# Kernel optimization log

Measured on AMD Instinct MI355X. Metric: run time of the kernel, lower is better.

## Reference

```python
import jax, jax.numpy as jnp
import numpy as np

B, S, D, H = 2, 2048, 2048, 16
HD = D // H
FF = 4 * D
EPS = 1e-5
SCALE = 1.0 / np.sqrt(D)  # source uses 1/sqrt(d_out), not 1/sqrt(head_dim)


def _gelu_tanh(x):
    c = np.sqrt(2.0 / np.pi).astype(np.float32)
    return 0.5 * x * (1.0 + jnp.tanh(c * (x + 0.044715 * x * x * x)))


def _layernorm(x, scale, shift):
    mean = jnp.mean(x, axis=-1, keepdims=True)
    var = jnp.mean(jnp.square(x - mean), axis=-1, keepdims=True)  # correction=0
    return (x - mean) * jax.lax.rsqrt(var + EPS) * scale + shift


def setup_inputs() -> dict:
    key = jax.random.key(0)
    ks = jax.random.split(key, 10)
    init = lambda k, shape, fan_in: (jax.random.normal(k, shape, jnp.float32) / np.sqrt(fan_in))
    return {
        "x": jax.random.normal(ks[0], (B, S, D), jnp.float32),
        "wq": init(ks[1], (D, D), D),
        "wk": init(ks[2], (D, D), D),
        "wv": init(ks[3], (D, D), D),
        "wo": init(ks[4], (D, D), D),
        "bo": jnp.zeros((D,), jnp.float32),
        "g1": jnp.ones((D,), jnp.float32),
        "s1": jnp.zeros((D,), jnp.float32),
        "g2": jnp.ones((D,), jnp.float32),
        "s2": jnp.zeros((D,), jnp.float32),
        "w1": init(ks[5], (D, FF), D),
        "b1": jnp.zeros((FF,), jnp.float32),
        "w2": init(ks[6], (FF, D), FF),
        "b2": jnp.zeros((D,), jnp.float32),
    }


def _block(x, wq, wk, wv, wo, bo, g1, s1, g2, s2, w1, b1, w2, b2):
    # pre-LN attention
    h = _layernorm(x, g1, s1)
    q = (h @ wq).reshape(B, S, H, HD).transpose(0, 2, 1, 3)  # [B,H,S,HD]
    k = (h @ wk).reshape(B, S, H, HD).transpose(0, 2, 1, 3)
    v = (h @ wv).reshape(B, S, H, HD).transpose(0, 2, 1, 3)
    scores = jnp.einsum('bhqd,bhkd->bhqk', q, k) * SCALE
    causal = jnp.tril(jnp.ones((S, S), dtype=bool))  # mask strictly-upper
    scores = jnp.where(causal, scores, -jnp.inf)
    attn = jax.nn.softmax(scores, axis=-1)
    ctx = jnp.einsum('bhqk,bhkd->bhqd', attn, v)
    ctx = ctx.transpose(0, 2, 1, 3).reshape(B, S, D)
    x = x + ctx @ wo + bo
    # pre-LN FFN
    h = _layernorm(x, g2, s2)
    h = _gelu_tanh(h @ w1 + b1) @ w2 + b2
    return x + h


def reference(x, wq, wk, wv, wo, bo, g1, s1, g2, s2, w1, b1, w2, b2):
    return _block(x, wq, wk, wv, wo, bo, g1, s1, g2, s2, w1, b1, w2, b2)
```

## Files before the change

### kernel.cpp

```cpp
#include <hip/hip_runtime.h>
#include <hip/hip_bf16.h>
#include <cstdint>

constexpr float SCALE_QK = 0.02209708691207961f;

using short8 = __attribute__((ext_vector_type(8))) short;
using f32x4  = __attribute__((ext_vector_type(4))) float;
using ushort4v = __attribute__((ext_vector_type(4))) ushort;

#define MFMA16(a,b,c) __builtin_amdgcn_mfma_f32_16x16x32_bf16((a),(b),(c),0,0,0)

__device__ __forceinline__ ushort f2bf(float f){
  uint32_t u = __builtin_bit_cast(uint32_t, f);
  u += 0x7fffu + ((u >> 16) & 1u);
  return (ushort)(u >> 16);
}

__device__ __forceinline__ void gload_lds16(const void* g, void* l){
  __builtin_amdgcn_global_load_lds(
      (const __attribute__((address_space(1))) void*)g,
      (__attribute__((address_space(3))) void*)l, 16, 0, 0);
}

#define VMCNT(n) asm volatile("s_waitcnt vmcnt(" #n ")" ::: "memory")
#define BAR() do{ __builtin_amdgcn_s_barrier(); \
  asm volatile("" ::: "memory"); \
  __builtin_amdgcn_sched_barrier(0); }while(0)

__global__ __launch_bounds__(256) void ln_kernel(
    const float* __restrict__ x, const float* __restrict__ g,
    const float* __restrict__ sh, ushort* __restrict__ out){
  const int row = blockIdx.x, t = threadIdx.x;
  const float* xr = x + (size_t)row*2048 + t*8;
  float v[8];
  *(float4*)&v[0] = *(const float4*)(xr);
  *(float4*)&v[4] = *(const float4*)(xr + 4);
  float s = 0.f, sq = 0.f;
#pragma unroll
  for (int i = 0; i < 8; ++i){ s += v[i]; sq += v[i]*v[i]; }
#pragma unroll
  for (int d = 1; d < 64; d <<= 1){ s += __shfl_xor(s, d, 64); sq += __shfl_xor(sq, d, 64); }
  __shared__ float red[8];
  const int w = t >> 6, lane = t & 63;
  if (lane == 0){ red[w] = s; red[4 + w] = sq; }
  __syncthreads();
  s  = red[0] + red[1] + red[2] + red[3];
  sq = red[4] + red[5] + red[6] + red[7];
  const float mean = s * (1.f/2048.f);
  const float inv  = rsqrtf(sq * (1.f/2048.f) - mean*mean + 1e-5f);
  union { ushort u[8]; uint4 v4; } o;
#pragma unroll
  for (int i = 0; i < 8; ++i){
    int j = t*8 + i;
    o.u[i] = f2bf((v[i] - mean) * inv * g[j] + sh[j]);
  }
  *(uint4*)(out + (size_t)row*2048 + t*8) = o.v4;
}

__global__ __launch_bounds__(256) void wconv_t(
    const float* __restrict__ in, ushort* __restrict__ out, int K, int N){
  __shared__ ushort tile[32][34];
  const int tx = threadIdx.x & 31, ty = threadIdx.x >> 5;
  const int n0 = blockIdx.x * 32, k0 = blockIdx.y * 32;
#pragma unroll
  for (int r = 0; r < 4; ++r){
    int kk = ty + r*8;
    tile[kk][tx] = f2bf(in[(size_t)(k0 + kk)*N + n0 + tx]);
  }
  __syncthreads();
#pragma unroll
  for (int r = 0; r < 4; ++r){
    int nn = ty + r*8;
    out[(size_t)(n0 + nn)*K + k0 + tx] = tile[tx][nn];
  }
}

#define MM(qd) do{ __builtin_amdgcn_s_setprio(1); \
  _Pragma("unroll") for (int mi = 0; mi < 4; ++mi) \
  _Pragma("unroll") for (int ni = 0; ni < 2; ++ni) \
  _Pragma("unroll") for (int kk = 0; kk < 2; ++kk) \
    acc[qd][mi][ni] = MFMA16(af[mi][kk], bf[ni][kk], acc[qd][mi][ni]); \
  __builtin_amdgcn_s_setprio(0); }while(0)

template<int EPI>
__global__ __launch_bounds__(512, 2) void gemm8p(
    const ushort* __restrict__ A, const ushort* __restrict__ Bt,
    int N, int K, void* __restrict__ outp, const float* __restrict__ bias){
  __shared__ ushort Al[2][2][128*64];
  __shared__ ushort Bl[2][2][128*64];
  const int tid = threadIdx.x, lane = tid & 63, wid = tid >> 6;
  const int l15 = lane & 15, l4 = lane >> 4;
  const int wrr = wid >> 2, wcc = wid & 3;

  const int bid = blockIdx.x;
  const int xcd = bid & 7, jj = bid >> 3;
  const int m0 = (xcd*2 + (jj & 1)) * 256;
  const int n0 = (jj >> 1) * 256;

  const ushort* Abase = A  + (size_t)m0*K;
  const ushort* Bbase = Bt + (size_t)n0*K;

  f32x4 acc[4][4][2];
#pragma unroll
  for (int q = 0; q < 4; ++q)
#pragma unroll
    for (int mi = 0; mi < 4; ++mi)
#pragma unroll
      for (int ni = 0; ni < 2; ++ni) acc[q][mi][ni] = (f32x4){0.f,0.f,0.f,0.f};

  auto stageA = [&](int buf, int h, int kt){
#pragma unroll
    for (int l = 0; l < 2; ++l){
      const int c = l*512 + tid, r = c >> 3, s = (c & 7) ^ ((c >> 3) & 7);
      gload_lds16(Abase + (size_t)(h*128 + r)*K + (size_t)kt*64 + s*8,
                  &Al[buf][h][c*8]);
    }
  };
  auto stageB = [&](int buf, int h, int kt){
#pragma unroll
    for (int l = 0; l < 2; ++l){
      const int c = l*512 + tid, r = c >> 3, s = (c & 7) ^ ((c >> 3) & 7);
      gload_lds16(Bbase + (size_t)(h*128 + r)*K + (size_t)kt*64 + s*8,
                  &Bl[buf][h][c*8]);
    }
  };

  short8 af[4][2], bf[2][2];
  auto readA = [&](int buf, int h){
#pragma unroll
    for (int mi = 0; mi < 4; ++mi){
      const int r = wrr*64 + mi*16 + l15;
#pragma unroll
      for (int kk = 0; kk < 2; ++kk)
        af[mi][kk] = *(const short8*)&Al[buf][h][r*64 + (((kk*4 + l4) ^ (r & 7))*8)];
    }
  };
  auto readB = [&](int buf, int h){
#pragma unroll
    for (int ni = 0; ni < 2; ++ni){
      const int r = wcc*32 + ni*16 + l15;
#pragma unroll
      for (int kk = 0; kk < 2; ++kk)
        bf[ni][kk] = *(const short8*)&Bl[buf][h][r*64 + (((kk*4 + l4) ^ (r & 7))*8)];
    }
  };

  const int NT = K >> 6;
  stageA(0,0,0); stageB(0,0,0); stageB(0,1,0); stageA(0,1,0);
  VMCNT(4); BAR();

  for (int kt = 0; kt < NT - 1; ++kt){
    const int cur = kt & 1, nxt = cur ^ 1;
    readA(cur,0); readB(cur,0);
    stageA(nxt,0,kt+1);
    VMCNT(4); BAR();
    MM(0); BAR();
    readB(cur,1);
    stageB(nxt,0,kt+1);
    VMCNT(4); BAR();
    MM(1); BAR();
    readA(cur,1);
    stageB(nxt,1,kt+1);
    BAR();
    MM(2); BAR();
    readB(cur,0);
    stageA(nxt,1,kt+1);
    VMCNT(4); BAR();
    MM(3); BAR();
  }
  {
    const int cur = (NT - 1) & 1;
    readA(cur,0); readB(cur,0); VMCNT(2); BAR(); MM(0); BAR();
    readB(cur,1);               VMCNT(0); BAR(); MM(1); BAR();
    readA(cur,1);                         BAR(); MM(2); BAR();
    readB(cur,0);                         BAR(); MM(3); BAR();
  }

#pragma unroll
  for (int qd = 0; qd < 4; ++qd){
    const int qr = qd >> 1, qc = qr ^ (qd & 1);
#pragma unroll
    for (int mi = 0; mi < 4; ++mi){
#pragma unroll
      for (int ni = 0; ni < 2; ++ni){
        const int mrow = m0 + qr*128 + wrr*64 + mi*16 + l4*4;
        const int col  = n0 + qc*128 + wcc*32 + ni*16 + l15;
        if constexpr (EPI == 0){
          const int which = col >> 11, rest = col & 2047;
          const int h = rest >> 7, d = rest & 127;
          const int b = mrow >> 11, s = mrow & 2047;
          if (which == 2){
            ushort4v o;
#pragma unroll
            for (int j2 = 0; j2 < 4; ++j2) o[j2] = f2bf(acc[qd][mi][ni][j2]);
            *(ushort4v*)&((ushort*)outp)[(size_t)2*8388608 +
                (size_t)(b*16 + h)*262144 + (size_t)d*2048 + s] = o;
          } else {
#pragma unroll
            for (int j2 = 0; j2 < 4; ++j2)
              ((ushort*)outp)[(size_t)which*8388608 +
                  (((size_t)(b*16 + h)*2048 + (s + j2)) << 7) + d] = f2bf(acc[qd][mi][ni][j2]);
          }
        } else {
#pragma unroll
          for (int j2 = 0; j2 < 4; ++j2){
            const float xx = acc[qd][mi][ni][j2] + bias[col];
            const float z  = 0.7978845608f*(xx + 0.044715f*xx*xx*xx);
            const float t  = __expf(-2.f*fabsf(z));
            const float th = (1.f - t)/(1.f + t);
            const float gl = 0.5f*xx*(1.f + copysignf(th, xx));
            ((ushort*)outp)[(size_t)(mrow + j2)*N + col] = f2bf(gl);
          }
        }
      }
    }
  }
}

template<int EPI>
__global__ __launch_bounds__(256) void gemm_bt(
    const ushort* __restrict__ A, const ushort* __restrict__ Bt,
    int N, int K, void* __restrict__ outp,
    const float* __restrict__ resid, const float* __restrict__ bias){
  __shared__ ushort lds[2][128*64];
  const int tid = threadIdx.x, lane = tid & 63, wid = tid >> 6;
  const int wr = wid >> 1, wc = wid & 1;
  const int l15 = lane & 15, l4 = lane >> 4;

  const int bid = blockIdx.x;
  const int xcd = bid & 7, j = bid >> 3;
  const int mb = xcd*4 + (j & 3);
  const int nb = j >> 2;
  const int m0 = mb * 128, n0 = nb * 128;

  f32x4 acc[4][4];
#pragma unroll
  for (int mi = 0; mi < 4; ++mi)
#pragma unroll
    for (int ni = 0; ni < 4; ++ni) acc[mi][ni] = (f32x4){0.f,0.f,0.f,0.f};

  const ushort* Abase = A  + (size_t)m0*K;
  const ushort* Bbase = Bt + (size_t)n0*K;

  const int NTk = K >> 6;
  for (int kt = 0; kt < NTk; ++kt){
    if (kt) __syncthreads();
#pragma unroll
    for (int i = 0; i < 4; ++i){
      const int chunk = (i*4 + wid)*64 + lane;
      const int row = chunk >> 3;
      const int c8  = (chunk & 7) ^ (row & 7);
      const size_t goff = (size_t)row*K + (size_t)kt*64 + c8*8;
      gload_lds16(Abase + goff, (ushort*)&lds[0][0] + (size_t)(i*4 + wid)*512);
      gload_lds16(Bbase + goff, (ushort*)&lds[1][0] + (size_t)(i*4 + wid)*512);
    }
    __syncthreads();

#pragma unroll
    for (int kk = 0; kk < 2; ++kk){
      short8 af[4], bf[4];
      const int kb = kk*4 + l4;
#pragma unroll
      for (int i = 0; i < 4; ++i){
        const int rA = wr*64 + i*16 + l15;
        af[i] = *(const short8*)&lds[0][rA*64 + ((kb ^ (rA & 7))*8)];
        const int rB = wc*64 + i*16 + l15;
        bf[i] = *(const short8*)&lds[1][rB*64 + ((kb ^ (rB & 7))*8)];
      }
#pragma unroll
      for (int mi = 0; mi < 4; ++mi)
#pragma unroll
        for (int ni = 0; ni < 4; ++ni)
          acc[mi][ni] = MFMA16(af[mi], bf[ni], acc[mi][ni]);
    }
  }

#pragma unroll
  for (int mi = 0; mi < 4; ++mi){
#pragma unroll
    for (int ni = 0; ni < 4; ++ni){
      const int rloc = wr*64 + mi*16 + l4*4;
      const int col  = n0 + wc*64 + ni*16 + l15;
#pragma unroll
      for (int j2 = 0; j2 < 4; ++j2){
        const int m = m0 + rloc + j2;
        float v = acc[mi][ni][j2];
        if constexpr (EPI == 1){
          ((float*)outp)[(size_t)m*N + col] = resid[(size_t)m*N + col] + bias[col] + v;
        } else {
          ((ushort*)outp)[(size_t)m*N + col] = f2bf(v);
        }
      }
    }
  }
}

__global__ __launch_bounds__(256, 2) void attn_kernel(
    const ushort* __restrict__ q, const ushort* __restrict__ k,
    const ushort* __restrict__ vt, ushort* __restrict__ ctx){
  __shared__ ushort k_lds[2][64*128];
  __shared__ ushort v_lds[2][128*64];
  __shared__ ushort p_lds[4][32*64];
  const int tid = threadIdx.x, lane = tid & 63, w = tid >> 6;
  const int l15 = lane & 15, l4 = lane >> 4;
  const int id = blockIdx.x;
  const int bh = id & 31;
  const int r  = id >> 5;
  const int qt = (r < 8) ? (15 - r) : (r - 8);
  const int bb = bh >> 4, hh = bh & 15;
  const ushort* kbase = k  + (size_t)bh * 262144;
  const ushort* vbase = vt + (size_t)bh * 262144;

  short8 qf[2][4];
#pragma unroll
  for (int mi = 0; mi < 2; ++mi){
    const int s = qt*128 + w*32 + mi*16 + l15;
    const ushort* qr = q + ((size_t)bh*2048 + s)*128 + l4*8;
#pragma unroll
    for (int kk = 0; kk < 4; ++kk) qf[mi][kk] = *(const short8*)(qr + kk*32);
  }

  f32x4 cacc[2][8];
#pragma unroll
  for (int mi = 0; mi < 2; ++mi)
#pragma unroll
    for (int dt = 0; dt < 8; ++dt) cacc[mi][dt] = (f32x4){0.f,0.f,0.f,0.f};
  float mrun[2][4], lrun[2][4];
#pragma unroll
  for (int mi = 0; mi < 2; ++mi)
#pragma unroll
    for (int j = 0; j < 4; ++j){ mrun[mi][j] = -1e30f; lrun[mi][j] = 0.f; }

  auto stage = [&](int buf, int t){
    const ushort* ksrc = kbase + (size_t)t*8192;
#pragma unroll
    for (int i = 0; i < 4; ++i){
      const int base = i*256 + w*64;
      const int chunk = base + lane;
      const int kr = chunk >> 4;
      const int c8 = (chunk & 15) ^ (kr & 7);
      gload_lds16(ksrc + (size_t)kr*128 + c8*8, &k_lds[buf][(size_t)base*8]);
    }
#pragma unroll
    for (int i = 0; i < 4; ++i){
      const int base = i*256 + w*64;
      const int chunk = base + lane;
      const int vr = chunk >> 3;
      const int c8 = (chunk & 7) ^ (vr & 7);
      gload_lds16(vbase + (size_t)vr*2048 + t*64 + c8*8, &v_lds[buf][(size_t)base*8]);
    }
  };

  const int nt = 2*qt + 2;
  stage(0, 0);
  __syncthreads();
  int cur = 0;
  for (int t = 0; t < nt; ++t){
    if (t + 1 < nt) stage(cur ^ 1, t + 1);

    f32x4 sa[2][4];
#pragma unroll
    for (int mi = 0; mi < 2; ++mi)
#pragma unroll
      for (int ct = 0; ct < 4; ++ct) sa[mi][ct] = (f32x4){0.f,0.f,0.f,0.f};
    __builtin_amdgcn_s_setprio(1);
#pragma unroll
    for (int kk = 0; kk < 4; ++kk){
#pragma unroll
      for (int ct = 0; ct < 4; ++ct){
        const int kr = ct*16 + l15;
        short8 kf = *(const short8*)&k_lds[cur][kr*128 + (((kk*4 + l4) ^ (kr & 7))*8)];
        sa[0][ct] = MFMA16(qf[0][kk], kf, sa[0][ct]);
        sa[1][ct] = MFMA16(qf[1][kk], kf, sa[1][ct]);
      }
    }
    __builtin_amdgcn_s_setprio(0);

    const bool diag = (t >= 2*qt);
#pragma unroll
    for (int mi = 0; mi < 2; ++mi){
#pragma unroll
      for (int j = 0; j < 4; ++j){
        const int qa = qt*128 + w*32 + mi*16 + l4*4 + j;
        float mnew = mrun[mi][j];
#pragma unroll
        for (int ct = 0; ct < 4; ++ct){
          float sc = sa[mi][ct][j] * SCALE_QK;
          if (diag){
            const int ka = t*64 + ct*16 + l15;
            sc = (ka > qa) ? -1e30f : sc;
          }
          sa[mi][ct][j] = sc;
          mnew = fmaxf(mnew, sc);
        }
#pragma unroll
        for (int d = 1; d < 16; d <<= 1) mnew = fmaxf(mnew, __shfl_xor(mnew, d, 16));
        const float corr = __expf(mrun[mi][j] - mnew);
        mrun[mi][j] = mnew; lrun[mi][j] *= corr;
        float psum = 0.f;
#pragma unroll
        for (int ct = 0; ct < 4; ++ct){
          const float p = __expf(sa[mi][ct][j] - mnew);
          sa[mi][ct][j] = p; psum += p;
        }
        lrun[mi][j] += psum;
#pragma unroll
        for (int dt = 0; dt < 8; ++dt) cacc[mi][dt][j] *= corr;
      }
    }

#pragma unroll
    for (int mi = 0; mi < 2; ++mi)
#pragma unroll
      for (int ct = 0; ct < 4; ++ct)
#pragma unroll
        for (int j = 0; j < 4; ++j){
          const int row = mi*16 + l4*4 + j, col = ct*16 + l15;
          p_lds[w][row*64 + ((col >> 3) ^ (row & 7))*8 + (col & 7)] = f2bf(sa[mi][ct][j]);
        }

    __builtin_amdgcn_s_setprio(1);
#pragma unroll
    for (int kk2 = 0; kk2 < 2; ++kk2){
      const int kb = kk2*4 + l4;
      short8 pa0 = *(const short8*)&p_lds[w][l15*64 + ((kb ^ (l15 & 7))*8)];
      short8 pa1 = *(const short8*)&p_lds[w][(16 + l15)*64 + ((kb ^ (l15 & 7))*8)];
#pragma unroll
      for (int dt = 0; dt < 8; ++dt){
        const int vr = dt*16 + l15;
        short8 vf = *(const short8*)&v_lds[cur][vr*64 + ((kb ^ (vr & 7))*8)];
        cacc[0][dt] = MFMA16(pa0, vf, cacc[0][dt]);
        cacc[1][dt] = MFMA16(pa1, vf, cacc[1][dt]);
      }
    }
    __builtin_amdgcn_s_setprio(0);

    if (t + 1 < nt){ __syncthreads(); cur ^= 1; }
  }

#pragma unroll
  for (int mi = 0; mi < 2; ++mi){
    float inv[4];
#pragma unroll
    for (int j = 0; j < 4; ++j){
      float lt = lrun[mi][j];
#pragma unroll
      for (int d = 1; d < 16; d <<= 1) lt += __shfl_xor(lt, d, 16);
      inv[j] = 1.f / lt;
    }
#pragma unroll
    for (int dt = 0; dt < 8; ++dt)
#pragma unroll
      for (int j = 0; j < 4; ++j){
        const int s = qt*128 + w*32 + mi*16 + l4*4 + j;
        const int d = dt*16 + l15;
        ctx[((size_t)(bb*2048 + s))*2048 + hh*128 + d] = f2bf(cacc[mi][dt][j] * inv[j]);
      }
  }
}

extern "C" void kernel_launch(void* const* d_in, const int* in_sizes, int n_in,
                              void* d_out, int out_size, void* d_ws, size_t ws_size,
                              hipStream_t stream) {
  const float* x  = (const float*)d_in[0];
  const float* wq = (const float*)d_in[1];
  const float* wk = (const float*)d_in[2];
  const float* wv = (const float*)d_in[3];
  const float* wo = (const float*)d_in[4];
  const float* bo = (const float*)d_in[5];
  const float* g1 = (const float*)d_in[6];
  const float* s1 = (const float*)d_in[7];
  const float* g2 = (const float*)d_in[8];
  const float* s2 = (const float*)d_in[9];
  const float* w1 = (const float*)d_in[10];
  const float* b1 = (const float*)d_in[11];
  const float* w2 = (const float*)d_in[12];
  const float* b2 = (const float*)d_in[13];
  float* out = (float*)d_out;
  char* ws = (char*)d_ws;

  ushort* wqkvT = (ushort*)(ws + 0);
  ushort* wkT = (ushort*)(ws + 8388608);
  ushort* wvT = (ushort*)(ws + 16777216);
  ushort* woT = (ushort*)(ws + 25165824);
  ushort* w1T = (ushort*)(ws + 33554432);
  ushort* w2T = (ushort*)(ws + 67108864);
  ushort* h1  = (ushort*)(ws + 100663296);
  ushort* qb  = (ushort*)(ws + 117440512);
  ushort* kb  = (ushort*)(ws + 134217728);
  ushort* vtb = (ushort*)(ws + 150994944);
  ushort* ctxb= (ushort*)(ws + 184549376);
  float*  x2  = (float*)(ws + 201326592);
  ushort* h2  = (ushort*)(ws + 234881024);
  ushort* ffb = (ushort*)(ws + 117440512);

  wconv_t<<<dim3(64, 64), 256, 0, stream>>>(wq, wqkvT, 2048, 2048);
  wconv_t<<<dim3(64, 64), 256, 0, stream>>>(wk, wkT, 2048, 2048);
  wconv_t<<<dim3(64, 64), 256, 0, stream>>>(wv, wvT, 2048, 2048);
  wconv_t<<<dim3(64, 64), 256, 0, stream>>>(wo, woT, 2048, 2048);
  wconv_t<<<dim3(256, 64), 256, 0, stream>>>(w1, w1T, 2048, 8192);
  wconv_t<<<dim3(64, 256), 256, 0, stream>>>(w2, w2T, 8192, 2048);

  ln_kernel<<<4096, 256, 0, stream>>>(x, g1, s1, h1);

  gemm8p<0><<<384, 512, 0, stream>>>(h1, wqkvT, 6144, 2048, qb, nullptr);

  attn_kernel<<<512, 256, 0, stream>>>(qb, kb, vtb, ctxb);

  gemm_bt<1><<<32*16, 256, 0, stream>>>(ctxb, woT, 2048, 2048, x2, x, bo);

  ln_kernel<<<4096, 256, 0, stream>>>(x2, g2, s2, h2);

  gemm8p<2><<<512, 512, 0, stream>>>(h2, w1T, 8192, 2048, ffb, b1);
  gemm_bt<1><<<32*16, 256, 0, stream>>>(ffb, w2T, 2048, 8192, out, x2, b2);

  (void)in_sizes; (void)n_in; (void)out_size; (void)ws_size;
}
```

Before: 754.4 us.

## Rework QKV GEMM epilogue, attention softmax, and merge weight conversions

Several changes land at once. Four square weight conversions are merged into one launch. The QKV projection moves from the 8-wave gemm8p to gemm_bt with an LDS-staged, coalesced epilogue that folds the QK scale and log2e into Q. The sched_barrier is dropped from the gemm8p barriers. In attention, fully masked diagonal sub-tiles are skipped per wave, masking is limited to waves that need it, softmax uses exp2, and the running-max rescale happens only when the max grows by more than a threshold (lazy rescaling). These target epilogue store inefficiency, redundant exp/mask work, and launch overhead, at the risk of different GEMM efficiency for the QKV shape and added numerical subtlety from lazy rescaling.

```diff
diff --git a/kernel.cpp b/kernel.cpp
--- a/kernel.cpp
+++ b/kernel.cpp
@@ -3,6 +3,7 @@
 #include <cstdint>
 
 constexpr float SCALE_QK = 0.02209708691207961f;
+constexpr float LOG2E    = 1.4426950408889634f;
 
 using short8 = __attribute__((ext_vector_type(8))) short;
 using f32x4  = __attribute__((ext_vector_type(4))) float;
@@ -23,9 +24,8 @@
 }
 
 #define VMCNT(n) asm volatile("s_waitcnt vmcnt(" #n ")" ::: "memory")
-#define BAR() do{ __builtin_amdgcn_s_barrier(); \
-  asm volatile("" ::: "memory"); \
-  __builtin_amdgcn_sched_barrier(0); }while(0)
+#define SBAR() do{ __builtin_amdgcn_s_barrier(); \
+  asm volatile("" ::: "memory"); }while(0)
 
 __global__ __launch_bounds__(256) void ln_kernel(
     const float* __restrict__ x, const float* __restrict__ g,
@@ -75,6 +75,28 @@
   }
 }
 
+__global__ __launch_bounds__(256) void wconv4(
+    const float* __restrict__ w0, const float* __restrict__ w1p,
+    const float* __restrict__ w2p, const float* __restrict__ w3p,
+    ushort* __restrict__ out){
+  __shared__ ushort tile[32][34];
+  const int tx = threadIdx.x & 31, ty = threadIdx.x >> 5;
+  const int n0 = blockIdx.x * 32, k0 = blockIdx.y * 32, z = blockIdx.z;
+  const float* in = (z == 0) ? w0 : (z == 1) ? w1p : (z == 2) ? w2p : w3p;
+  ushort* o = out + (size_t)z * 4194304;
+#pragma unroll
+  for (int r = 0; r < 4; ++r){
+    int kk = ty + r*8;
+    tile[kk][tx] = f2bf(in[(size_t)(k0 + kk)*2048 + n0 + tx]);
+  }
+  __syncthreads();
+#pragma unroll
+  for (int r = 0; r < 4; ++r){
+    int nn = ty + r*8;
+    o[(size_t)(n0 + nn)*2048 + k0 + tx] = tile[tx][nn];
+  }
+}
+
 #define MM(qd) do{ __builtin_amdgcn_s_setprio(1); \
   _Pragma("unroll") for (int mi = 0; mi < 4; ++mi) \
   _Pragma("unroll") for (int ni = 0; ni < 2; ++ni) \
@@ -147,33 +169,33 @@
 
   const int NT = K >> 6;
   stageA(0,0,0); stageB(0,0,0); stageB(0,1,0); stageA(0,1,0);
-  VMCNT(4); BAR();
+  VMCNT(4); SBAR();
 
   for (int kt = 0; kt < NT - 1; ++kt){
     const int cur = kt & 1, nxt = cur ^ 1;
     readA(cur,0); readB(cur,0);
     stageA(nxt,0,kt+1);
-    VMCNT(4); BAR();
-    MM(0); BAR();
+    VMCNT(4); SBAR();
+    MM(0); SBAR();
     readB(cur,1);
     stageB(nxt,0,kt+1);
-    VMCNT(4); BAR();
-    MM(1); BAR();
+    VMCNT(4); SBAR();
+    MM(1); SBAR();
     readA(cur,1);
     stageB(nxt,1,kt+1);
-    BAR();
-    MM(2); BAR();
+    SBAR();
+    MM(2); SBAR();
     readB(cur,0);
     stageA(nxt,1,kt+1);
-    VMCNT(4); BAR();
-    MM(3); BAR();
+    VMCNT(4); SBAR();
+    MM(3); SBAR();
   }
   {
     const int cur = (NT - 1) & 1;
-    readA(cur,0); readB(cur,0); VMCNT(2); BAR(); MM(0); BAR();
-    readB(cur,1);               VMCNT(0); BAR(); MM(1); BAR();
-    readA(cur,1);                         BAR(); MM(2); BAR();
-    readB(cur,0);                         BAR(); MM(3); BAR();
+    readA(cur,0); readB(cur,0); VMCNT(2); SBAR(); MM(0); SBAR();
+    readB(cur,1);               VMCNT(0); SBAR(); MM(1); SBAR();
+    readA(cur,1);                         SBAR(); MM(2); SBAR();
+    readB(cur,0);                         SBAR(); MM(3); SBAR();
   }
 
 #pragma unroll
@@ -185,32 +207,14 @@
       for (int ni = 0; ni < 2; ++ni){
         const int mrow = m0 + qr*128 + wrr*64 + mi*16 + l4*4;
         const int col  = n0 + qc*128 + wcc*32 + ni*16 + l15;
-        if constexpr (EPI == 0){
-          const int which = col >> 11, rest = col & 2047;
-          const int h = rest >> 7, d = rest & 127;
-          const int b = mrow >> 11, s = mrow & 2047;
-          if (which == 2){
-            ushort4v o;
-#pragma unroll
-            for (int j2 = 0; j2 < 4; ++j2) o[j2] = f2bf(acc[qd][mi][ni][j2]);
-            *(ushort4v*)&((ushort*)outp)[(size_t)2*8388608 +
-                (size_t)(b*16 + h)*262144 + (size_t)d*2048 + s] = o;
-          } else {
-#pragma unroll
-            for (int j2 = 0; j2 < 4; ++j2)
-              ((ushort*)outp)[(size_t)which*8388608 +
-                  (((size_t)(b*16 + h)*2048 + (s + j2)) << 7) + d] = f2bf(acc[qd][mi][ni][j2]);
-          }
-        } else {
-#pragma unroll
-          for (int j2 = 0; j2 < 4; ++j2){
-            const float xx = acc[qd][mi][ni][j2] + bias[col];
-            const float z  = 0.7978845608f*(xx + 0.044715f*xx*xx*xx);
-            const float t  = __expf(-2.f*fabsf(z));
-            const float th = (1.f - t)/(1.f + t);
-            const float gl = 0.5f*xx*(1.f + copysignf(th, xx));
-            ((ushort*)outp)[(size_t)(mrow + j2)*N + col] = f2bf(gl);
-          }
+#pragma unroll
+        for (int j2 = 0; j2 < 4; ++j2){
+          const float xx = acc[qd][mi][ni][j2] + bias[col];
+          const float z  = 0.7978845608f*(xx + 0.044715f*xx*xx*xx);
+          const float t  = __expf(-2.f*fabsf(z));
+          const float th = (1.f - t)/(1.f + t);
+          const float gl = 0.5f*xx*(1.f + copysignf(th, xx));
+          ((ushort*)outp)[(size_t)(mrow + j2)*N + col] = f2bf(gl);
         }
       }
     }
@@ -275,20 +279,74 @@
     }
   }
 
-#pragma unroll
-  for (int mi = 0; mi < 4; ++mi){
-#pragma unroll
-    for (int ni = 0; ni < 4; ++ni){
-      const int rloc = wr*64 + mi*16 + l4*4;
-      const int col  = n0 + wc*64 + ni*16 + l15;
-#pragma unroll
-      for (int j2 = 0; j2 < 4; ++j2){
-        const int m = m0 + rloc + j2;
-        float v = acc[mi][ni][j2];
-        if constexpr (EPI == 1){
-          ((float*)outp)[(size_t)m*N + col] = resid[(size_t)m*N + col] + bias[col] + v;
-        } else {
-          ((ushort*)outp)[(size_t)m*N + col] = f2bf(v);
+  if constexpr (EPI == 0){
+    __syncthreads();
+    ushort* tile = (ushort*)&lds[0][0];
+    const int which = n0 >> 11;
+    const int hh = (n0 & 2047) >> 7;
+    const int bb = m0 >> 11, srow0 = m0 & 2047;
+    if (which != 2){
+      const float qs = (which == 0) ? SCALE_QK * LOG2E : 1.0f;
+#pragma unroll
+      for (int mi = 0; mi < 4; ++mi)
+#pragma unroll
+        for (int ni = 0; ni < 4; ++ni){
+          const int rl = wr*64 + mi*16 + l4*4;
+          const int cl = wc*64 + ni*16 + l15;
+#pragma unroll
+          for (int j2 = 0; j2 < 4; ++j2)
+            tile[(rl + j2)*128 + cl] = f2bf(acc[mi][ni][j2] * qs);
+        }
+      __syncthreads();
+      ushort* dst = (ushort*)outp + (size_t)which*8388608 +
+                    ((size_t)(bb*16 + hh)*2048 + srow0)*128;
+#pragma unroll
+      for (int i = 0; i < 8; ++i){
+        const int c = i*256 + tid, row = c >> 4, d8 = (c & 15)*8;
+        *(uint4*)(dst + (size_t)row*128 + d8) = *(const uint4*)&tile[row*128 + d8];
+      }
+    } else {
+#pragma unroll
+      for (int mi = 0; mi < 4; ++mi)
+#pragma unroll
+        for (int ni = 0; ni < 4; ++ni){
+          const int rl = wr*64 + mi*16 + l4*4;
+          const int cl = wc*64 + ni*16 + l15;
+          ushort4v o;
+#pragma unroll
+          for (int j2 = 0; j2 < 4; ++j2) o[j2] = f2bf(acc[mi][ni][j2]);
+          *(ushort4v*)&tile[cl*128 + rl] = o;
+        }
+      __syncthreads();
+      ushort* dst = (ushort*)outp + (size_t)2*8388608 +
+                    (size_t)(bb*16 + hh)*262144 + srow0;
+#pragma unroll
+      for (int i = 0; i < 8; ++i){
+        const int c = i*256 + tid, drow = c >> 4, s8 = (c & 15)*8;
+        *(uint4*)(dst + (size_t)drow*2048 + s8) = *(const uint4*)&tile[drow*128 + s8];
+      }
+    }
+  } else {
+#pragma unroll
+    for (int mi = 0; mi < 4; ++mi){
+#pragma unroll
+      for (int ni = 0; ni < 4; ++ni){
+        const int rloc = wr*64 + mi*16 + l4*4;
+        const int col  = n0 + wc*64 + ni*16 + l15;
+#pragma unroll
+        for (int j2 = 0; j2 < 4; ++j2){
+          const int m = m0 + rloc + j2;
+          float v = acc[mi][ni][j2];
+          if constexpr (EPI == 1){
+            ((float*)outp)[(size_t)m*N + col] = resid[(size_t)m*N + col] + bias[col] + v;
+          } else {
+            const float xx = v + bias[col];
+            const float z  = 0.7978845608f*(xx + 0.044715f*xx*xx*xx);
+            const float t  = __expf(-2.f*fabsf(z));
+            const float th = (1.f - t)/(1.f + t);
+            const float gl = 0.5f*xx*(1.f + copysignf(th, xx));
+            ((ushort*)outp)[(size_t)m*N + col] = f2bf(gl);
+          }
         }
       }
     }
@@ -358,82 +416,102 @@
   for (int t = 0; t < nt; ++t){
     if (t + 1 < nt) stage(cur ^ 1, t + 1);
 
-    f32x4 sa[2][4];
-#pragma unroll
-    for (int mi = 0; mi < 2; ++mi)
-#pragma unroll
-      for (int ct = 0; ct < 4; ++ct) sa[mi][ct] = (f32x4){0.f,0.f,0.f,0.f};
-    __builtin_amdgcn_s_setprio(1);
-#pragma unroll
-    for (int kk = 0; kk < 4; ++kk){
-#pragma unroll
-      for (int ct = 0; ct < 4; ++ct){
-        const int kr = ct*16 + l15;
-        short8 kf = *(const short8*)&k_lds[cur][kr*128 + (((kk*4 + l4) ^ (kr & 7))*8)];
-        sa[0][ct] = MFMA16(qf[0][kk], kf, sa[0][ct]);
-        sa[1][ct] = MFMA16(qf[1][kk], kf, sa[1][ct]);
-      }
-    }
-    __builtin_amdgcn_s_setprio(0);
-
-    const bool diag = (t >= 2*qt);
-#pragma unroll
-    for (int mi = 0; mi < 2; ++mi){
-#pragma unroll
-      for (int j = 0; j < 4; ++j){
-        const int qa = qt*128 + w*32 + mi*16 + l4*4 + j;
-        float mnew = mrun[mi][j];
+    const bool skip = (t == 2*qt + 1) && (w < 2);
+    if (!skip){
+      f32x4 sa[2][4];
+#pragma unroll
+      for (int mi = 0; mi < 2; ++mi)
+#pragma unroll
+        for (int ct = 0; ct < 4; ++ct) sa[mi][ct] = (f32x4){0.f,0.f,0.f,0.f};
+      __builtin_amdgcn_s_setprio(1);
+#pragma unroll
+      for (int kk = 0; kk < 4; ++kk){
 #pragma unroll
         for (int ct = 0; ct < 4; ++ct){
-          float sc = sa[mi][ct][j] * SCALE_QK;
-          if (diag){
-            const int ka = t*64 + ct*16 + l15;
-            sc = (ka > qa) ? -1e30f : sc;
+          const int kr = ct*16 + l15;
+          short8 kf = *(const short8*)&k_lds[cur][kr*128 + (((kk*4 + l4) ^ (kr & 7))*8)];
+          sa[0][ct] = MFMA16(qf[0][kk], kf, sa[0][ct]);
+          sa[1][ct] = MFMA16(qf[1][kk], kf, sa[1][ct]);
+        }
+      }
+      __builtin_amdgcn_s_setprio(0);
+
+      const bool anymask = (t >= 2*qt) && !((t == 2*qt) && (w >= 2));
+      float rowmax[2][4];
+      bool grow = false;
+#pragma unroll
+      for (int mi = 0; mi < 2; ++mi){
+#pragma unroll
+        for (int j = 0; j < 4; ++j){
+          const int qa = qt*128 + w*32 + mi*16 + l4*4 + j;
+          float mx = -1e30f;
+#pragma unroll
+          for (int ct = 0; ct < 4; ++ct){
+            float sc = sa[mi][ct][j];
+            if (anymask){
+              const int ka = t*64 + ct*16 + l15;
+              sc = (ka > qa) ? -1e30f : sc;
+            }
+            sa[mi][ct][j] = sc;
+            mx = fmaxf(mx, sc);
           }
-          sa[mi][ct][j] = sc;
-          mnew = fmaxf(mnew, sc);
-        }
-#pragma unroll
-        for (int d = 1; d < 16; d <<= 1) mnew = fmaxf(mnew, __shfl_xor(mnew, d, 16));
-        const float corr = __expf(mrun[mi][j] - mnew);
-        mrun[mi][j] = mnew; lrun[mi][j] *= corr;
-        float psum = 0.f;
-#pragma unroll
-        for (int ct = 0; ct < 4; ++ct){
-          const float p = __expf(sa[mi][ct][j] - mnew);
-          sa[mi][ct][j] = p; psum += p;
-        }
-        lrun[mi][j] += psum;
-#pragma unroll
-        for (int dt = 0; dt < 8; ++dt) cacc[mi][dt][j] *= corr;
-      }
-    }
-
-#pragma unroll
-    for (int mi = 0; mi < 2; ++mi)
-#pragma unroll
-      for (int ct = 0; ct < 4; ++ct)
+#pragma unroll
+          for (int d = 1; d < 16; d <<= 1) mx = fmaxf(mx, __shfl_xor(mx, d, 16));
+          rowmax[mi][j] = mx;
+          grow = grow || (mx > mrun[mi][j] + 8.f);
+        }
+      }
+      if (__any(grow)){
+#pragma unroll
+        for (int mi = 0; mi < 2; ++mi)
+#pragma unroll
+          for (int j = 0; j < 4; ++j){
+            const float mnew = fmaxf(mrun[mi][j], rowmax[mi][j]);
+            const float corr = exp2f(mrun[mi][j] - mnew);
+            mrun[mi][j] = mnew; lrun[mi][j] *= corr;
+#pragma unroll
+            for (int dt = 0; dt < 8; ++dt) cacc[mi][dt][j] *= corr;
+          }
+      }
+#pragma unroll
+      for (int mi = 0; mi < 2; ++mi)
 #pragma unroll
         for (int j = 0; j < 4; ++j){
-          const int row = mi*16 + l4*4 + j, col = ct*16 + l15;
-          p_lds[w][row*64 + ((col >> 3) ^ (row & 7))*8 + (col & 7)] = f2bf(sa[mi][ct][j]);
-        }
-
-    __builtin_amdgcn_s_setprio(1);
-#pragma unroll
-    for (int kk2 = 0; kk2 < 2; ++kk2){
-      const int kb = kk2*4 + l4;
-      short8 pa0 = *(const short8*)&p_lds[w][l15*64 + ((kb ^ (l15 & 7))*8)];
-      short8 pa1 = *(const short8*)&p_lds[w][(16 + l15)*64 + ((kb ^ (l15 & 7))*8)];
-#pragma unroll
-      for (int dt = 0; dt < 8; ++dt){
-        const int vr = dt*16 + l15;
-        short8 vf = *(const short8*)&v_lds[cur][vr*64 + ((kb ^ (vr & 7))*8)];
-        cacc[0][dt] = MFMA16(pa0, vf, cacc[0][dt]);
-        cacc[1][dt] = MFMA16(pa1, vf, cacc[1][dt]);
-      }
-    }
-    __builtin_amdgcn_s_setprio(0);
+          float psum = 0.f;
+#pragma unroll
+          for (int ct = 0; ct < 4; ++ct){
+            const float p = exp2f(sa[mi][ct][j] - mrun[mi][j]);
+            sa[mi][ct][j] = p; psum += p;
+          }
+          lrun[mi][j] += psum;
+        }
+
+#pragma unroll
+      for (int mi = 0; mi < 2; ++mi)
+#pragma unroll
+        for (int ct = 0; ct < 4; ++ct)
+#pragma unroll
+          for (int j = 0; j < 4; ++j){
+            const int row = mi*16 + l4*4 + j, col = ct*16 + l15;
+            p_lds[w][row*64 + ((col >> 3) ^ (row & 7))*8 + (col & 7)] = f2bf(sa[mi][ct][j]);
+          }
+
+      __builtin_amdgcn_s_setprio(1);
+#pragma unroll
+      for (int kk2 = 0; kk2 < 2; ++kk2){
+        const int kb = kk2*4 + l4;
+        short8 pa0 = *(const short8*)&p_lds[w][l15*64 + ((kb ^ (l15 & 7))*8)];
+        short8 pa1 = *(const short8*)&p_lds[w][(16 + l15)*64 + ((kb ^ (l15 & 7))*8)];
+#pragma unroll
+        for (int dt = 0; dt < 8; ++dt){
+          const int vr = dt*16 + l15;
+          short8 vf = *(const short8*)&v_lds[cur][vr*64 + ((kb ^ (vr & 7))*8)];
+          cacc[0][dt] = MFMA16(pa0, vf, cacc[0][dt]);
+          cacc[1][dt] = MFMA16(pa1, vf, cacc[1][dt]);
+        }
+      }
+      __builtin_amdgcn_s_setprio(0);
+    }
 
     if (t + 1 < nt){ __syncthreads(); cur ^= 1; }
   }
@@ -480,8 +558,6 @@
   char* ws = (char*)d_ws;
 
   ushort* wqkvT = (ushort*)(ws + 0);
-  ushort* wkT = (ushort*)(ws + 8388608);
-  ushort* wvT = (ushort*)(ws + 16777216);
   ushort* woT = (ushort*)(ws + 25165824);
   ushort* w1T = (ushort*)(ws + 33554432);
   ushort* w2T = (ushort*)(ws + 67108864);
@@ -494,16 +570,13 @@
   ushort* h2  = (ushort*)(ws + 234881024);
   ushort* ffb = (ushort*)(ws + 117440512);
 
-  wconv_t<<<dim3(64, 64), 256, 0, stream>>>(wq, wqkvT, 2048, 2048);
-  wconv_t<<<dim3(64, 64), 256, 0, stream>>>(wk, wkT, 2048, 2048);
-  wconv_t<<<dim3(64, 64), 256, 0, stream>>>(wv, wvT, 2048, 2048);
-  wconv_t<<<dim3(64, 64), 256, 0, stream>>>(wo, woT, 2048, 2048);
+  wconv4<<<dim3(64, 64, 4), 256, 0, stream>>>(wq, wk, wv, wo, wqkvT);
   wconv_t<<<dim3(256, 64), 256, 0, stream>>>(w1, w1T, 2048, 8192);
   wconv_t<<<dim3(64, 256), 256, 0, stream>>>(w2, w2T, 8192, 2048);
 
   ln_kernel<<<4096, 256, 0, stream>>>(x, g1, s1, h1);
 
-  gemm8p<0><<<384, 512, 0, stream>>>(h1, wqkvT, 6144, 2048, qb, nullptr);
+  gemm_bt<0><<<32*48, 256, 0, stream>>>(h1, wqkvT, 6144, 2048, qb, nullptr, nullptr);
 
   attn_kernel<<<512, 256, 0, stream>>>(qb, kb, vtb, ctxb);
 
```

Result: faster. 708.2 us (-6.1%).
